# Kernel tuning notes

Measured on AMD Instinct MI355X. Metric: run time of the kernel, lower is better.

## Reference

```python
import jax, jax.numpy as jnp
import numpy as np

H = 8          # num_heads
CHUNK = 68     # tokens_per_chunk = blocks_per_chunk(4) * tokens_per_block(17)
EPS = 1e-5


def _layer_norm(t, w, b):
    m = t.mean(-1, keepdims=True)
    v = t.var(-1, keepdims=True)
    return (t - m) / jnp.sqrt(v + EPS) * w + b


def _forward(tokens, embedding, Wq, bq, Wk, bk, Wv, bv, Wg, bg, Wo, bo,
             gn_w, gn_b, ln1_w, ln1_b, ln2_w, ln2_b, w1, b1, w2, b2):
    B, S = tokens.shape
    L, D, _ = Wq.shape
    dh = D // H
    n_chunks = S // CHUNK

    x = embedding[tokens]  # [B,S,D]

    # per-head decay gammas (standard RetNet)
    gamma = 1.0 - 2.0 ** (-5.0 - jnp.arange(H, dtype=jnp.float32))  # [H]

    # rotary relative-position tables (absolute positions, fresh state n=0)
    pos = jnp.arange(S, dtype=jnp.float32)
    inv = 1.0 / (10000.0 ** (jnp.arange(0, dh, 2, dtype=jnp.float32) / dh))
    ang = pos[:, None] * inv[None, :]                      # [S, dh/2]
    cs = jnp.concatenate([jnp.cos(ang)] * 2, -1)[None, :, None, :]  # [1,S,1,dh]
    sn = jnp.concatenate([jnp.sin(ang)] * 2, -1)[None, :, None, :]

    def rot(t):  # t: [B,S,H,dh]
        t1, t2 = jnp.split(t, 2, axis=-1)
        return t * cs + jnp.concatenate([-t2, t1], -1) * sn

    # chunkwise decay structures
    idx = jnp.arange(CHUNK, dtype=jnp.float32)
    expo = idx[:, None] - idx[None, :]
    Dmask = jnp.where(expo >= 0, gamma[:, None, None] ** expo[None], 0.0)  # [H,C,C]
    cross_dec = gamma[None, :] ** (idx[:, None] + 1.0)          # [C,H]
    k_dec = gamma[None, :] ** (CHUNK - 1.0 - idx[:, None])      # [C,H]
    chunk_dec = gamma ** CHUNK                                  # [H]

    for l in range(L):
        h = _layer_norm(x, ln1_w[l], ln1_b[l])
        q = rot((h @ Wq[l] + bq[l]).reshape(B, S, H, dh))
        k = rot((h @ Wk[l] + bk[l]).reshape(B, S, H, dh)) * (dh ** -0.5)
        v = (h @ Wv[l] + bv[l]).reshape(B, S, H, dh)
        # split into chunks, scan carries the per-head KV state [B,H,dh,dh]
        qc = q.reshape(B, n_chunks, CHUNK, H, dh).transpose(1, 0, 2, 3, 4)
        kc = k.reshape(B, n_chunks, CHUNK, H, dh).transpose(1, 0, 2, 3, 4)
        vc = v.reshape(B, n_chunks, CHUNK, H, dh).transpose(1, 0, 2, 3, 4)

        def step(state, qkv):
            qq, kk, vv = qkv  # each [B,C,H,dh]
            inner = jnp.einsum('bihd,bjhd->bhij', qq, kk) * Dmask
            out = jnp.einsum('bhij,bjhd->bihd', inner, vv)
            out = out + jnp.einsum('bihd,bhde->bihe', qq, state) * cross_dec[None, :, :, None]
            state = state * chunk_dec[None, :, None, None] + \
                jnp.einsum('bjhd,bjhe->bhde', kk * k_dec[None, :, :, None], vv)
            return state, out

        state0 = jnp.zeros((B, H, dh, dh), dtype=x.dtype)
        _, ret = jax.lax.scan(step, state0, (qc, kc, vc))
        ret = ret.transpose(1, 0, 2, 3, 4).reshape(B, S, H, dh)
        # per-head group norm
        m = ret.mean(-1, keepdims=True)
        vr = ret.var(-1, keepdims=True)
        ret = (ret - m) / jnp.sqrt(vr + EPS)
        ret = (ret * gn_w[l].reshape(H, dh) + gn_b[l].reshape(H, dh)).reshape(B, S, D)
        g = jax.nn.silu(h @ Wg[l] + bg[l])
        x = x + (g * ret) @ Wo[l] + bo[l]
        h2 = _layer_norm(x, ln2_w[l], ln2_b[l])
        x = x + jax.nn.silu(h2 @ w1[l] + b1[l]) @ w2[l] + b2[l]
    return x


def setup_inputs() -> dict:
    key = jax.random.key(0)
    B, S, D, L, FF, V = 16, 408, 512, 10, 2048, 519
    ks = jax.random.split(key, 16)
    r = lambda i, shape, s=0.02: jax.random.normal(ks[i], shape, dtype=jnp.float32) * s
    return {
        'tokens': jax.random.randint(ks[0], (B, S), 0, V, dtype=jnp.int32),
        'embedding': r(1, (V, D)),
        'Wq': r(2, (L, D, D)), 'bq': jnp.zeros((L, D), jnp.float32),
        'Wk': r(3, (L, D, D)), 'bk': jnp.zeros((L, D), jnp.float32),
        'Wv': r(4, (L, D, D)), 'bv': jnp.zeros((L, D), jnp.float32),
        'Wg': r(5, (L, D, D)), 'bg': jnp.zeros((L, D), jnp.float32),
        'Wo': r(6, (L, D, D)), 'bo': jnp.zeros((L, D), jnp.float32),
        'gn_w': jnp.ones((L, D), jnp.float32), 'gn_b': jnp.zeros((L, D), jnp.float32),
        'ln1_w': jnp.ones((L, D), jnp.float32), 'ln1_b': jnp.zeros((L, D), jnp.float32),
        'ln2_w': jnp.ones((L, D), jnp.float32), 'ln2_b': jnp.zeros((L, D), jnp.float32),
        'w1': r(7, (L, D, FF)), 'b1': jnp.zeros((L, FF), jnp.float32),
        'w2': r(8, (L, FF, D)), 'b2': jnp.zeros((L, D), jnp.float32),
    }


def reference(tokens, embedding, Wq, bq, Wk, bk, Wv, bv, Wg, bg, Wo, bo,
              gn_w, gn_b, ln1_w, ln1_b, ln2_w, ln2_b, w1, b1, w2, b2):
    return _forward(tokens, embedding, Wq, bq, Wk, bk, Wv, bv, Wg, bg, Wo, bo,
                    gn_w, gn_b, ln1_w, ln1_b, ln2_w, ln2_b, w1, b1, w2, b2)
```

## Files before the change

kernel.cpp:

```cpp
#include <hip/hip_runtime.h>
#include <hip/hip_bf16.h>

#define H 8
#define DH 64
#define DMODEL 512
#define SEQ 408
#define BATCH 16
#define NLAYER 10
#define FFDIM 2048
#define CHUNK 68
#define NCHUNK 6
#define M (BATCH*SEQ)
#define EPS 1e-5f

typedef __hip_bfloat16 bf16;
typedef unsigned short ushort_t;
typedef short bf8v __attribute__((ext_vector_type(8)));
typedef float f4v  __attribute__((ext_vector_type(4)));

static constexpr size_t QKVG_STRIDE = 2u*512*512;
static constexpr size_t QKVG_HL     = 512*512;
static constexpr size_t WO_HI = 0;
static constexpr size_t WO_LO = WO_HI + 512*512;
static constexpr size_t W1_HI = WO_LO + 512*512;
static constexpr size_t W1_LO = W1_HI + 2048*512;
static constexpr size_t W2_HI = W1_LO + 2048*512;
static constexpr size_t W2_LO = W2_HI + 512*2048;

__device__ __forceinline__ float us2f(unsigned short u){ return __uint_as_float(((unsigned)u) << 16); }
__device__ __forceinline__ unsigned short f2bfs(float f){
  __bf16 h = (__bf16)f;
  return *(unsigned short*)&h;
}
__device__ __forceinline__ void split2(float f, unsigned short& hi, unsigned short& lo){
  hi = f2bfs(f);
  lo = f2bfs(f - us2f(hi));
}

typedef const __attribute__((address_space(1))) unsigned int* gas_ptr;
typedef __attribute__((address_space(3))) unsigned int* las_ptr;
__device__ __forceinline__ void gld16(const void* g, void* l){
  __builtin_amdgcn_global_load_lds((gas_ptr)g, (las_ptr)l, 16, 0, 0);
}

__device__ __forceinline__ int xcd_swz(int fid, int nwg){
  int q = nwg >> 3;
  return (fid & 7) * q + (fid >> 3);
}

__global__ void embed_kernel(const int* __restrict__ tokens, const float* __restrict__ emb,
                             float* __restrict__ x){
  int idx = blockIdx.x*256 + threadIdx.x;
  if (idx >= M*DMODEL) return;
  int r = idx >> 9; int d = idx & 511;
  x[idx] = emb[(size_t)tokens[r]*DMODEL + d];
}

__global__ __launch_bounds__(256) void ln_kernel(const float* __restrict__ x,
    const float* __restrict__ w, const float* __restrict__ b,
    ushort_t* __restrict__ hhi, ushort_t* __restrict__ hlo){
  __shared__ float red[8];
  int r = blockIdx.x, tid = threadIdx.x;
  size_t base = (size_t)r*DMODEL;
  float v0 = x[base + tid], v1 = x[base + tid + 256];
  float s = v0 + v1, s2 = v0*v0 + v1*v1;
  int lane = tid & 63, wv = tid >> 6;
  #pragma unroll
  for (int o = 32; o; o >>= 1){ s += __shfl_xor(s, o); s2 += __shfl_xor(s2, o); }
  if (lane == 0){ red[wv] = s; red[wv+4] = s2; }
  __syncthreads();
  float tot  = red[0]+red[1]+red[2]+red[3];
  float tot2 = red[4]+red[5]+red[6]+red[7];
  float mean = tot * (1.0f/512.0f);
  float var  = tot2 * (1.0f/512.0f) - mean*mean;
  float rinv = rsqrtf(var + EPS);
  float o0 = (v0-mean)*rinv*w[tid]     + b[tid];
  float o1 = (v1-mean)*rinv*w[tid+256] + b[tid+256];
  unsigned short hi, lo;
  split2(o0, hi, lo); hhi[base+tid] = hi; hlo[base+tid] = lo;
  split2(o1, hi, lo); hhi[base+tid+256] = hi; hlo[base+tid+256] = lo;
}

__device__ __forceinline__ void wsplit_tile(const float* __restrict__ W,
    ushort_t* __restrict__ hi, ushort_t* __restrict__ lo,
    int N, int K, int n0, int k0)
{
  __shared__ float tb[32][33];
  int tx = threadIdx.x & 31, ty = threadIdx.x >> 5;
  #pragma unroll
  for (int r = 0; r < 32; r += 8)
    tb[ty+r][tx] = W[(size_t)(k0+ty+r)*N + n0 + tx];
  __syncthreads();
  #pragma unroll
  for (int r = 0; r < 32; r += 8){
    float v = tb[tx][ty+r];
    unsigned short h, l; split2(v, h, l);
    size_t o = (size_t)(n0+ty+r)*K + k0 + tx;
    hi[o] = h; lo[o] = l;
  }
}

__global__ __launch_bounds__(256) void wsplit_qkvg_kernel(
    const float* __restrict__ Wq, const float* __restrict__ Wk,
    const float* __restrict__ Wv, const float* __restrict__ Wg,
    ushort_t* __restrict__ wsp)
{
  int z = blockIdx.z;
  const float* W = (z==0)?Wq:(z==1)?Wk:(z==2)?Wv:Wg;
  ushort_t* hi = wsp + (size_t)z*QKVG_STRIDE;
  wsplit_tile(W, hi, hi + QKVG_HL, 512, 512, blockIdx.x*32, blockIdx.y*32);
}

__global__ __launch_bounds__(256) void wsplit_ffo_kernel(
    const float* __restrict__ Wo, const float* __restrict__ w1,
    const float* __restrict__ w2, ushort_t* __restrict__ wsp)
{
  int b = blockIdx.x;
  const float* W; ushort_t* hi; int N, K, n0, k0;
  if (b < 256){
    W = Wo; hi = wsp + WO_HI; N = 512; K = 512;
    n0 = (b & 15)*32; k0 = (b >> 4)*32;
  } else if (b < 1280){
    int bb = b - 256;
    W = w1; hi = wsp + W1_HI; N = 2048; K = 512;
    n0 = (bb & 63)*32; k0 = (bb >> 6)*32;
  } else {
    int bb = b - 1280;
    W = w2; hi = wsp + W2_HI; N = 512; K = 2048;
    n0 = (bb & 15)*32; k0 = (bb >> 4)*32;
  }
  wsplit_tile(W, hi, hi + (size_t)N*K, N, K, n0, k0);
}

#define BK 32

#define STAGE_PS(buf, kofs) do{ \
    gld16(aHp + (kofs), &AsH[buf][tid*8]); \
    gld16(aLp + (kofs), &AsL[buf][tid*8]); \
    gld16(bHp + (kofs), &BsH[buf][tid*8]); \
    gld16(bLp + (kofs), &BsL[buf][tid*8]); \
    gld16(bHp2 + (kofs), &BsH[buf][tid*8 + 2048]); \
    gld16(bLp2 + (kofs), &BsL[buf][tid*8 + 2048]); \
  }while(0)

__global__ __launch_bounds__(256) void gemm_ps_kernel(
    const ushort_t* __restrict__ Ahi, const ushort_t* __restrict__ Alo,
    const ushort_t* __restrict__ Bhi, const ushort_t* __restrict__ Blo,
    const float* __restrict__ bias,
    const float* Cin, float* Cout, ushort_t* Co_hi, ushort_t* Co_lo,
    int N, int K, int epi)
{
  __shared__ __align__(16) short AsH[2][64*BK];
  __shared__ __align__(16) short AsL[2][64*BK];
  __shared__ __align__(16) short BsH[2][128*BK];
  __shared__ __align__(16) short BsL[2][128*BK];
  int tid = threadIdx.x;
  int lane = tid & 63, wave = tid >> 6;
  int wm = (wave >> 1) * 32, wn = (wave & 1) * 64;
  int l15 = lane & 15, quad = lane >> 4;

  int nwg = gridDim.x * gridDim.y;
  int fid = blockIdx.y * gridDim.x + blockIdx.x;
  int swz = xcd_swz(fid, nwg);
  int bn = (swz % gridDim.x) * 128;
  int bm = (swz / gridDim.x) * 64;

  f4v acc[2][4];
  #pragma unroll
  for (int i = 0; i < 2; i++)
    #pragma unroll
    for (int j = 0; j < 4; j++) acc[i][j] = (f4v){0.f,0.f,0.f,0.f};

  int arow = tid >> 2, ak = (tid & 3) * 8;
  const ushort_t* aHp  = Ahi + (size_t)(bm + arow)*K + ak;
  const ushort_t* aLp  = Alo + (size_t)(bm + arow)*K + ak;
  const ushort_t* bHp  = Bhi + (size_t)(bn + arow)*K + ak;
  const ushort_t* bLp  = Blo + (size_t)(bn + arow)*K + ak;
  const ushort_t* bHp2 = Bhi + (size_t)(bn + 64 + arow)*K + ak;
  const ushort_t* bLp2 = Blo + (size_t)(bn + 64 + arow)*K + ak;

  STAGE_PS(0, 0);
  const int nt = K / BK;
  for (int t = 0; t < nt; t++){
    __syncthreads();
    if (t + 1 < nt) STAGE_PS((t+1)&1, (t+1)*BK);
    int cur = t & 1;
    bf8v afh[2], afl[2], bfh[4], bfl[4];
    #pragma unroll
    for (int i = 0; i < 2; i++){
      afh[i] = *(const bf8v*)&AsH[cur][(wm + i*16 + l15)*BK + quad*8];
      afl[i] = *(const bf8v*)&AsL[cur][(wm + i*16 + l15)*BK + quad*8];
    }
    #pragma unroll
    for (int j = 0; j < 4; j++){
      bfh[j] = *(const bf8v*)&BsH[cur][(wn + j*16 + l15)*BK + quad*8];
      bfl[j] = *(const bf8v*)&BsL[cur][(wn + j*16 + l15)*BK + quad*8];
    }
    #pragma unroll
    for (int i = 0; i < 2; i++)
      #pragma unroll
      for (int j = 0; j < 4; j++){
        acc[i][j] = __builtin_amdgcn_mfma_f32_16x16x32_bf16(afh[i], bfl[j], acc[i][j], 0, 0, 0);
        acc[i][j] = __builtin_amdgcn_mfma_f32_16x16x32_bf16(afl[i], bfh[j], acc[i][j], 0, 0, 0);
        acc[i][j] = __builtin_amdgcn_mfma_f32_16x16x32_bf16(afh[i], bfh[j], acc[i][j], 0, 0, 0);
      }
  }
  #pragma unroll
  for (int i = 0; i < 2; i++){
    int m0 = bm + wm + i*16 + quad*4;
    #pragma unroll
    for (int j = 0; j < 4; j++){
      int n = bn + wn + j*16 + l15;
      float bsv = bias[n];
      #pragma unroll
      for (int r = 0; r < 4; r++){
        int m = m0 + r;
        float c = acc[i][j][r] + bsv;
        if (epi == 1) c = c / (1.0f + expf(-c));
        if (epi == 2) c += Cin[(size_t)m*N + n];
        if (Co_hi){
          unsigned short hi, lo; split2(c, hi, lo);
          Co_hi[(size_t)m*N + n] = hi;
          Co_lo[(size_t)m*N + n] = lo;
        } else {
          Cout[(size_t)m*N + n] = c;
        }
      }
    }
  }
}

__global__ __launch_bounds__(256) void gemm_qkvg_kernel(
    const ushort_t* __restrict__ Ahi, const ushort_t* __restrict__ Alo,
    const ushort_t* __restrict__ wsp,
    const float* __restrict__ bq, const float* __restrict__ bk,
    const float* __restrict__ bv, const float* __restrict__ bg,
    float* __restrict__ qo, float* __restrict__ ko,
    float* __restrict__ vo, float* __restrict__ go)
{
  const int N = DMODEL, K = DMODEL;
  __shared__ __align__(16) short AsH[2][64*BK];
  __shared__ __align__(16) short AsL[2][64*BK];
  __shared__ __align__(16) short BsH[2][128*BK];
  __shared__ __align__(16) short BsL[2][128*BK];
  int tid = threadIdx.x;
  int lane = tid & 63, wave = tid >> 6;
  int wm = (wave >> 1) * 32, wn = (wave & 1) * 64;
  int l15 = lane & 15, quad = lane >> 4;

  int nwg = gridDim.x * gridDim.y;
  int fid = blockIdx.y * gridDim.x + blockIdx.x;
  int swz = xcd_swz(fid, nwg);
  int bx = swz % gridDim.x;
  int which = bx >> 2;
  int bn = (bx & 3) * 128;
  int bm = (swz / gridDim.x) * 64;

  const ushort_t* Bhi = wsp + (size_t)which * QKVG_STRIDE;
  const ushort_t* Blo = Bhi + QKVG_HL;
  const float* bias = (which==0) ? bq : (which==1) ? bk : (which==2) ? bv : bg;
  float* out        = (which==0) ? qo : (which==1) ? ko : (which==2) ? vo : go;

  f4v acc[2][4];
  #pragma unroll
  for (int i = 0; i < 2; i++)
    #pragma unroll
    for (int j = 0; j < 4; j++) acc[i][j] = (f4v){0.f,0.f,0.f,0.f};

  int arow = tid >> 2, ak = (tid & 3) * 8;
  const ushort_t* aHp  = Ahi + (size_t)(bm + arow)*K + ak;
  const ushort_t* aLp  = Alo + (size_t)(bm + arow)*K + ak;
  const ushort_t* bHp  = Bhi + (size_t)(bn + arow)*K + ak;
  const ushort_t* bLp  = Blo + (size_t)(bn + arow)*K + ak;
  const ushort_t* bHp2 = Bhi + (size_t)(bn + 64 + arow)*K + ak;
  const ushort_t* bLp2 = Blo + (size_t)(bn + 64 + arow)*K + ak;

  STAGE_PS(0, 0);
  const int nt = K / BK;
  for (int t = 0; t < nt; t++){
    __syncthreads();
    if (t + 1 < nt) STAGE_PS((t+1)&1, (t+1)*BK);
    int cur = t & 1;
    bf8v afh[2], afl[2], bfh[4], bfl[4];
    #pragma unroll
    for (int i = 0; i < 2; i++){
      afh[i] = *(const bf8v*)&AsH[cur][(wm + i*16 + l15)*BK + quad*8];
      afl[i] = *(const bf8v*)&AsL[cur][(wm + i*16 + l15)*BK + quad*8];
    }
    #pragma unroll
    for (int j = 0; j < 4; j++){
      bfh[j] = *(const bf8v*)&BsH[cur][(wn + j*16 + l15)*BK + quad*8];
      bfl[j] = *(const bf8v*)&BsL[cur][(wn + j*16 + l15)*BK + quad*8];
    }
    #pragma unroll
    for (int i = 0; i < 2; i++)
      #pragma unroll
      for (int j = 0; j < 4; j++){
        acc[i][j] = __builtin_amdgcn_mfma_f32_16x16x32_bf16(afh[i], bfl[j], acc[i][j], 0, 0, 0);
        acc[i][j] = __builtin_amdgcn_mfma_f32_16x16x32_bf16(afl[i], bfh[j], acc[i][j], 0, 0, 0);
        acc[i][j] = __builtin_amdgcn_mfma_f32_16x16x32_bf16(afh[i], bfh[j], acc[i][j], 0, 0, 0);
      }
  }
  #pragma unroll
  for (int i = 0; i < 2; i++){
    int m0 = bm + wm + i*16 + quad*4;
    #pragma unroll
    for (int j = 0; j < 4; j++){
      int n = bn + wn + j*16 + l15;
      float bsv = bias[n];
      #pragma unroll
      for (int r = 0; r < 4; r++){
        int m = m0 + r;
        float c = acc[i][j][r] + bsv;
        if (which == 3) c = c / (1.0f + expf(-c));
        out[(size_t)m*N + n] = c;
      }
    }
  }
}

__global__ void rope_kernel(float* __restrict__ q, float* __restrict__ k){
  int idx = blockIdx.x*256 + threadIdx.x;
  if (idx >= M*256) return;
  int r = idx >> 8, p = idx & 255;
  int hh = p >> 5, i = p & 31;
  int s = r % SEQ;
  float inv = powf(10000.0f, -(float)(2*i) * (1.0f/64.0f));
  float ang = (float)s * inv;
  float sn, c; sincosf(ang, &sn, &c);
  size_t base = (size_t)r*DMODEL + hh*64 + i;
  float q1 = q[base], q2 = q[base+32];
  q[base]    = q1*c - q2*sn;
  q[base+32] = q2*c + q1*sn;
  float k1 = k[base], k2 = k[base+32];
  const float sc = 0.125f;
  k[base]    = (k1*c - k2*sn)*sc;
  k[base+32] = (k2*c + k1*sn)*sc;
}

__global__ __launch_bounds__(256) void ret_chunkkv_kernel(
    const float* __restrict__ k, const float* __restrict__ v, float* __restrict__ Ast)
{
  __shared__ __align__(16) float kT[DH][CHUNK];
  __shared__ __align__(16) float vs[CHUNK][DH];
  __shared__ float gpw[CHUNK];
  int tid = threadIdx.x;
  int c = blockIdx.x % NCHUNK;
  int bh = blockIdx.x / NCHUNK;
  int hh = bh & 7, b = bh >> 3;
  float gamma = 1.0f - exp2f(-5.0f - (float)hh);
  if (tid < CHUNK) gpw[tid] = powf(gamma, (float)(CHUNK-1-tid));
  size_t rowbase = ((size_t)(b*SEQ + c*CHUNK))*DMODEL + hh*DH;
  for (int e = tid; e < CHUNK*DH; e += 256){
    int i = e >> 6, d = e & 63;
    size_t g = rowbase + (size_t)i*DMODEL + d;
    kT[d][i] = k[g];
    vs[i][d] = v[g];
  }
  __syncthreads();
  float* A = Ast + (size_t)blockIdx.x * (DH*DH);
  for (int e = tid; e < DH*16; e += 256){
    int d = e >> 4, q4 = (e & 15) * 4;
    float4 a4 = {0,0,0,0};
    for (int j = 0; j < CHUNK; j++){
      float kj = kT[d][j] * gpw[j];
      float4 v4 = *(const float4*)&vs[j][q4];
      a4.x += kj*v4.x; a4.y += kj*v4.y; a4.z += kj*v4.z; a4.w += kj*v4.w;
    }
    *(float4*)&A[d*DH + q4] = a4;
  }
}

__global__ __launch_bounds__(256) void ret_scan_kernel(float* __restrict__ Ast)
{
  int bh = blockIdx.x, hh = bh & 7;
  float gamma = 1.0f - exp2f(-5.0f - (float)hh);
  float chdec = powf(gamma, (float)CHUNK);
  int tid = threadIdx.x;
  float4 run[4];
  #pragma unroll
  for (int t = 0; t < 4; t++) run[t] = (float4){0,0,0,0};
  size_t base = (size_t)bh * NCHUNK * (DH*DH) + (size_t)tid*16;
  for (int c = 0; c < NCHUNK; c++){
    float4* slot = (float4*)(Ast + base + (size_t)c*(DH*DH));
    float4 a[4];
    #pragma unroll
    for (int t = 0; t < 4; t++) a[t] = slot[t];
    #pragma unroll
    for (int t = 0; t < 4; t++) slot[t] = run[t];
    #pragma unroll
    for (int t = 0; t < 4; t++){
      run[t].x = run[t].x*chdec + a[t].x;
      run[t].y = run[t].y*chdec + a[t].y;
      run[t].z = run[t].z*chdec + a[t].z;
      run[t].w = run[t].w*chdec + a[t].w;
    }
  }
}

__global__ __launch_bounds__(256) void ret_out_kernel(
    const float* __restrict__ q, const float* __restrict__ k, const float* __restrict__ v,
    const float* __restrict__ Ast, float* __restrict__ ret)
{
  __shared__ __align__(16) float qs[CHUNK][DH];
  __shared__ __align__(16) float kT[DH][CHUNK];
  __shared__ __align__(16) float vs[CHUNK][DH];
  __shared__ __align__(16) float sts[DH*DH];
  __shared__ float inner[34][CHUNK];
  __shared__ float gpw[CHUNK];
  int tid = threadIdx.x;
  int c = blockIdx.x % NCHUNK;
  int bh = blockIdx.x / NCHUNK;
  int hh = bh & 7, b = bh >> 3;
  float gamma = 1.0f - exp2f(-5.0f - (float)hh);
  if (tid < CHUNK) gpw[tid] = powf(gamma, (float)tid);
  size_t rowbase = ((size_t)(b*SEQ + c*CHUNK))*DMODEL + hh*DH;
  for (int e = tid; e < CHUNK*DH; e += 256){
    int i = e >> 6, d = e & 63;
    size_t g = rowbase + (size_t)i*DMODEL + d;
    qs[i][d] = q[g];
    kT[d][i] = k[g];
    vs[i][d] = v[g];
  }
  const float* st = Ast + (size_t)blockIdx.x * (DH*DH);
  for (int e = tid*4; e < DH*DH; e += 1024)
    *(float4*)&sts[e] = *(const float4*)&st[e];
  __syncthreads();
  for (int p = 0; p < 2; p++){
    int i0 = p*34;
    for (int e = tid; e < 34*CHUNK; e += 256){
      int ii = e / CHUNK, j = e - ii*CHUNK;
      int i = i0 + ii;
      float val = 0.0f;
      if (j <= i){
        float dot = 0.0f;
        #pragma unroll 16
        for (int d = 0; d < DH; d++) dot += qs[i][d] * kT[d][j];
        val = dot * gpw[i-j];
      }
      inner[ii][j] = val;
    }
    __syncthreads();
    for (int e = tid; e < 34*16; e += 256){
      int ii = e >> 4, q4 = (e & 15) * 4;
      int i = i0 + ii;
      float4 o4 = {0,0,0,0};
      for (int j = 0; j <= i; j++){
        float w = inner[ii][j];
        float4 v4 = *(const float4*)&vs[j][q4];
        o4.x += w*v4.x; o4.y += w*v4.y; o4.z += w*v4.z; o4.w += w*v4.w;
      }
      float4 c4 = {0,0,0,0};
      #pragma unroll 8
      for (int e2 = 0; e2 < DH; e2++){
        float qv = qs[i][e2];
        float4 s4 = *(const float4*)&sts[e2*DH + q4];
        c4.x += qv*s4.x; c4.y += qv*s4.y; c4.z += qv*s4.z; c4.w += qv*s4.w;
      }
      float cd = gpw[i] * gamma;
      size_t ob = rowbase + (size_t)i*DMODEL + q4;
      float4 o; o.x = o4.x + cd*c4.x; o.y = o4.y + cd*c4.y;
      o.z = o4.z + cd*c4.z; o.w = o4.w + cd*c4.w;
      *(float4*)&ret[ob] = o;
    }
    __syncthreads();
  }
}

__global__ __launch_bounds__(512) void gnorm_gate_kernel(const float* __restrict__ ret,
    const float* __restrict__ g, const float* __restrict__ gnw, const float* __restrict__ gnb,
    ushort_t* __restrict__ ohi, ushort_t* __restrict__ olo)
{
  int r = blockIdx.x, tid = threadIdx.x;
  size_t idx = (size_t)r*DMODEL + tid;
  float val = ret[idx];
  float s = val, s2 = val*val;
  #pragma unroll
  for (int o = 32; o; o >>= 1){ s += __shfl_xor(s, o); s2 += __shfl_xor(s2, o); }
  float mean = s * (1.0f/64.0f);
  float var  = s2 * (1.0f/64.0f) - mean*mean;
  float y = (val - mean) * rsqrtf(var + EPS);
  y = y * gnw[tid] + gnb[tid];
  y = y * g[idx];
  unsigned short hi, lo; split2(y, hi, lo);
  ohi[idx] = hi; olo[idx] = lo;
}

__global__ void outwrite_kernel(const float* __restrict__ x, float* __restrict__ out){
  int idx = blockIdx.x*256 + threadIdx.x;
  if (idx < M*DMODEL) out[idx] = x[idx];
}

extern "C" void kernel_launch(void* const* d_in, const int* in_sizes, int n_in,
                              void* d_out, int out_size, void* d_ws, size_t ws_size,
                              hipStream_t stream)
{
  (void)in_sizes; (void)n_in; (void)out_size; (void)ws_size;
  const int*   tokens = (const int*)d_in[0];
  const float* emb  = (const float*)d_in[1];
  const float* Wq = (const float*)d_in[2];  const float* bq = (const float*)d_in[3];
  const float* Wk = (const float*)d_in[4];  const float* bk = (const float*)d_in[5];
  const float* Wv = (const float*)d_in[6];  const float* bv = (const float*)d_in[7];
  const float* Wg = (const float*)d_in[8];  const float* bg = (const float*)d_in[9];
  const float* Wo = (const float*)d_in[10]; const float* bo = (const float*)d_in[11];
  const float* gnw = (const float*)d_in[12]; const float* gnb = (const float*)d_in[13];
  const float* ln1w = (const float*)d_in[14]; const float* ln1b = (const float*)d_in[15];
  const float* ln2w = (const float*)d_in[16]; const float* ln2b = (const float*)d_in[17];
  const float* w1 = (const float*)d_in[18]; const float* b1 = (const float*)d_in[19];
  const float* w2 = (const float*)d_in[20]; const float* b2 = (const float*)d_in[21];

  const size_t MD = (size_t)M*DMODEL;
  float* xf = (float*)d_ws;
  float* qf = xf + MD;
  float* kf = qf + MD;
  float* vf = kf + MD;
  float* gf = vf + MD;
  float* rf = gf + MD;
  ushort_t* h_hi = (ushort_t*)(rf + MD);
  ushort_t* h_lo = h_hi + MD;
  float* Ast = (float*)h_hi;
  ushort_t* rg_hi = h_hi;
  ushort_t* rg_lo = h_lo;
  ushort_t* ff_hi = (ushort_t*)qf;
  ushort_t* ff_lo = (ushort_t*)vf;
  ushort_t* wsp = (ushort_t*)rf;

  embed_kernel<<<(M*DMODEL)/256, 256, 0, stream>>>(tokens, emb, xf);

  dim3 gqkvg(16, M/64);
  dim3 g512(DMODEL/128, M/64);
  dim3 gff(FFDIM/128, M/64);
  dim3 gsplit4(16, 16, 4);
  for (int l = 0; l < NLAYER; l++){
    const size_t wO = (size_t)l*DMODEL*DMODEL;
    const size_t bO = (size_t)l*DMODEL;
    const size_t w1O = (size_t)l*DMODEL*FFDIM;
    const size_t b1O = (size_t)l*FFDIM;
    wsplit_qkvg_kernel<<<gsplit4, 256, 0, stream>>>(Wq + wO, Wk + wO, Wv + wO, Wg + wO, wsp);
    ln_kernel<<<M, 256, 0, stream>>>(xf, ln1w + bO, ln1b + bO, h_hi, h_lo);
    gemm_qkvg_kernel<<<gqkvg, 256, 0, stream>>>(h_hi, h_lo, wsp,
        bq + bO, bk + bO, bv + bO, bg + bO,
        qf, kf, vf, gf);
    rope_kernel<<<M, 256, 0, stream>>>(qf, kf);
    ret_chunkkv_kernel<<<BATCH*H*NCHUNK, 256, 0, stream>>>(kf, vf, Ast);
    ret_scan_kernel<<<BATCH*H, 256, 0, stream>>>(Ast);
    ret_out_kernel<<<BATCH*H*NCHUNK, 256, 0, stream>>>(qf, kf, vf, Ast, rf);
    gnorm_gate_kernel<<<M, 512, 0, stream>>>(rf, gf, gnw + bO, gnb + bO, rg_hi, rg_lo);
    wsplit_ffo_kernel<<<2304, 256, 0, stream>>>(Wo + wO, w1 + w1O, w2 + w1O, wsp);
    gemm_ps_kernel<<<g512, 256, 0, stream>>>(rg_hi, rg_lo,
        wsp + WO_HI, wsp + WO_LO, bo + bO, xf, xf, nullptr, nullptr, DMODEL, DMODEL, 2);
    ln_kernel<<<M, 256, 0, stream>>>(xf, ln2w + bO, ln2b + bO, h_hi, h_lo);
    gemm_ps_kernel<<<gff, 256, 0, stream>>>(h_hi, h_lo,
        wsp + W1_HI, wsp + W1_LO, b1 + b1O, nullptr, nullptr, ff_hi, ff_lo, FFDIM, DMODEL, 1);
    gemm_ps_kernel<<<g512, 256, 0, stream>>>(ff_hi, ff_lo,
        wsp + W2_HI, wsp + W2_LO, b2 + bO, xf, xf, nullptr, nullptr, DMODEL, FFDIM, 2);
  }
  outwrite_kernel<<<(M*DMODEL)/256, 256, 0, stream>>>(xf, (float*)d_out);
}
```

Measured before the change: 3.767 ms.

## Deepen GEMM prefetch to two tiles and use 64-wide N tiles for 512-out GEMMs

Restructures the bf16-split GEMM main loops so two K-tiles are in flight. Explicit vmcnt waits and split barriers let the next-next tile load while the current tile computes, replacing a single sync per iteration. The output-projection and FFN-down GEMMs are templated to use a 64-column N tile, which doubles their workgroup count for better occupancy and CU fill. This adds a second barrier per iteration and relies on hand-counted vmcnt values that must match the number of issued loads.

```diff
diff --git a/kernel.cpp b/kernel.cpp
--- a/kernel.cpp
+++ b/kernel.cpp
@@ -134,15 +134,7 @@
 
 #define BK 32
 
-#define STAGE_PS(buf, kofs) do{ \
-    gld16(aHp + (kofs), &AsH[buf][tid*8]); \
-    gld16(aLp + (kofs), &AsL[buf][tid*8]); \
-    gld16(bHp + (kofs), &BsH[buf][tid*8]); \
-    gld16(bLp + (kofs), &BsL[buf][tid*8]); \
-    gld16(bHp2 + (kofs), &BsH[buf][tid*8 + 2048]); \
-    gld16(bLp2 + (kofs), &BsL[buf][tid*8 + 2048]); \
-  }while(0)
-
+template<int TBN>
 __global__ __launch_bounds__(256) void gemm_ps_kernel(
     const ushort_t* __restrict__ Ahi, const ushort_t* __restrict__ Alo,
     const ushort_t* __restrict__ Bhi, const ushort_t* __restrict__ Blo,
@@ -150,26 +142,27 @@
     const float* Cin, float* Cout, ushort_t* Co_hi, ushort_t* Co_lo,
     int N, int K, int epi)
 {
+  constexpr int TNW = TBN/32;
   __shared__ __align__(16) short AsH[2][64*BK];
   __shared__ __align__(16) short AsL[2][64*BK];
-  __shared__ __align__(16) short BsH[2][128*BK];
-  __shared__ __align__(16) short BsL[2][128*BK];
+  __shared__ __align__(16) short BsH[2][TBN*BK];
+  __shared__ __align__(16) short BsL[2][TBN*BK];
   int tid = threadIdx.x;
   int lane = tid & 63, wave = tid >> 6;
-  int wm = (wave >> 1) * 32, wn = (wave & 1) * 64;
+  int wm = (wave >> 1) * 32, wn = (wave & 1) * (TBN/2);
   int l15 = lane & 15, quad = lane >> 4;
 
   int nwg = gridDim.x * gridDim.y;
   int fid = blockIdx.y * gridDim.x + blockIdx.x;
   int swz = xcd_swz(fid, nwg);
-  int bn = (swz % gridDim.x) * 128;
+  int bn = (swz % gridDim.x) * TBN;
   int bm = (swz / gridDim.x) * 64;
 
-  f4v acc[2][4];
+  f4v acc[2][TNW];
   #pragma unroll
   for (int i = 0; i < 2; i++)
     #pragma unroll
-    for (int j = 0; j < 4; j++) acc[i][j] = (f4v){0.f,0.f,0.f,0.f};
+    for (int j = 0; j < TNW; j++) acc[i][j] = (f4v){0.f,0.f,0.f,0.f};
 
   int arow = tid >> 2, ak = (tid & 3) * 8;
   const ushort_t* aHp  = Ahi + (size_t)(bm + arow)*K + ak;
@@ -179,37 +172,59 @@
   const ushort_t* bHp2 = Bhi + (size_t)(bn + 64 + arow)*K + ak;
   const ushort_t* bLp2 = Blo + (size_t)(bn + 64 + arow)*K + ak;
 
-  STAGE_PS(0, 0);
+  auto STAGE = [&](int buf, int kofs){
+    gld16(aHp + kofs, &AsH[buf][tid*8]);
+    gld16(aLp + kofs, &AsL[buf][tid*8]);
+    gld16(bHp + kofs, &BsH[buf][tid*8]);
+    gld16(bLp + kofs, &BsL[buf][tid*8]);
+    if constexpr (TBN == 128){
+      gld16(bHp2 + kofs, &BsH[buf][tid*8 + 2048]);
+      gld16(bLp2 + kofs, &BsL[buf][tid*8 + 2048]);
+    }
+  };
+
+  STAGE(0, 0);
+  STAGE(1, BK);
   const int nt = K / BK;
   for (int t = 0; t < nt; t++){
-    __syncthreads();
-    if (t + 1 < nt) STAGE_PS((t+1)&1, (t+1)*BK);
+    if (t + 1 < nt){
+      if constexpr (TBN == 128) asm volatile("s_waitcnt vmcnt(6)" ::: "memory");
+      else                      asm volatile("s_waitcnt vmcnt(4)" ::: "memory");
+    } else {
+      asm volatile("s_waitcnt vmcnt(0)" ::: "memory");
+    }
+    __builtin_amdgcn_s_barrier();
+    asm volatile("" ::: "memory");
     int cur = t & 1;
-    bf8v afh[2], afl[2], bfh[4], bfl[4];
+    bf8v afh[2], afl[2], bfh[TNW], bfl[TNW];
     #pragma unroll
     for (int i = 0; i < 2; i++){
       afh[i] = *(const bf8v*)&AsH[cur][(wm + i*16 + l15)*BK + quad*8];
       afl[i] = *(const bf8v*)&AsL[cur][(wm + i*16 + l15)*BK + quad*8];
     }
     #pragma unroll
-    for (int j = 0; j < 4; j++){
+    for (int j = 0; j < TNW; j++){
       bfh[j] = *(const bf8v*)&BsH[cur][(wn + j*16 + l15)*BK + quad*8];
       bfl[j] = *(const bf8v*)&BsL[cur][(wn + j*16 + l15)*BK + quad*8];
     }
     #pragma unroll
     for (int i = 0; i < 2; i++)
       #pragma unroll
-      for (int j = 0; j < 4; j++){
+      for (int j = 0; j < TNW; j++){
         acc[i][j] = __builtin_amdgcn_mfma_f32_16x16x32_bf16(afh[i], bfl[j], acc[i][j], 0, 0, 0);
         acc[i][j] = __builtin_amdgcn_mfma_f32_16x16x32_bf16(afl[i], bfh[j], acc[i][j], 0, 0, 0);
         acc[i][j] = __builtin_amdgcn_mfma_f32_16x16x32_bf16(afh[i], bfh[j], acc[i][j], 0, 0, 0);
       }
+    asm volatile("s_waitcnt lgkmcnt(0)" ::: "memory");
+    __builtin_amdgcn_s_barrier();
+    asm volatile("" ::: "memory");
+    if (t + 2 < nt) STAGE(cur, (t+2)*BK);
   }
   #pragma unroll
   for (int i = 0; i < 2; i++){
     int m0 = bm + wm + i*16 + quad*4;
     #pragma unroll
-    for (int j = 0; j < 4; j++){
+    for (int j = 0; j < TNW; j++){
       int n = bn + wn + j*16 + l15;
       float bsv = bias[n];
       #pragma unroll
@@ -275,11 +290,23 @@
   const ushort_t* bHp2 = Bhi + (size_t)(bn + 64 + arow)*K + ak;
   const ushort_t* bLp2 = Blo + (size_t)(bn + 64 + arow)*K + ak;
 
-  STAGE_PS(0, 0);
+  auto STAGE = [&](int buf, int kofs){
+    gld16(aHp + kofs, &AsH[buf][tid*8]);
+    gld16(aLp + kofs, &AsL[buf][tid*8]);
+    gld16(bHp + kofs, &BsH[buf][tid*8]);
+    gld16(bLp + kofs, &BsL[buf][tid*8]);
+    gld16(bHp2 + kofs, &BsH[buf][tid*8 + 2048]);
+    gld16(bLp2 + kofs, &BsL[buf][tid*8 + 2048]);
+  };
+
+  STAGE(0, 0);
+  STAGE(1, BK);
   const int nt = K / BK;
   for (int t = 0; t < nt; t++){
-    __syncthreads();
-    if (t + 1 < nt) STAGE_PS((t+1)&1, (t+1)*BK);
+    if (t + 1 < nt) asm volatile("s_waitcnt vmcnt(6)" ::: "memory");
+    else            asm volatile("s_waitcnt vmcnt(0)" ::: "memory");
+    __builtin_amdgcn_s_barrier();
+    asm volatile("" ::: "memory");
     int cur = t & 1;
     bf8v afh[2], afl[2], bfh[4], bfl[4];
     #pragma unroll
@@ -300,6 +327,10 @@
         acc[i][j] = __builtin_amdgcn_mfma_f32_16x16x32_bf16(afl[i], bfh[j], acc[i][j], 0, 0, 0);
         acc[i][j] = __builtin_amdgcn_mfma_f32_16x16x32_bf16(afh[i], bfh[j], acc[i][j], 0, 0, 0);
       }
+    asm volatile("s_waitcnt lgkmcnt(0)" ::: "memory");
+    __builtin_amdgcn_s_barrier();
+    asm volatile("" ::: "memory");
+    if (t + 2 < nt) STAGE(cur, (t+2)*BK);
   }
   #pragma unroll
   for (int i = 0; i < 2; i++){
@@ -528,7 +559,7 @@
   embed_kernel<<<(M*DMODEL)/256, 256, 0, stream>>>(tokens, emb, xf);
 
   dim3 gqkvg(16, M/64);
-  dim3 g512(DMODEL/128, M/64);
+  dim3 g512(DMODEL/64, M/64);
   dim3 gff(FFDIM/128, M/64);
   dim3 gsplit4(16, 16, 4);
   for (int l = 0; l < NLAYER; l++){
@@ -547,12 +578,12 @@
     ret_out_kernel<<<BATCH*H*NCHUNK, 256, 0, stream>>>(qf, kf, vf, Ast, rf);
     gnorm_gate_kernel<<<M, 512, 0, stream>>>(rf, gf, gnw + bO, gnb + bO, rg_hi, rg_lo);
     wsplit_ffo_kernel<<<2304, 256, 0, stream>>>(Wo + wO, w1 + w1O, w2 + w1O, wsp);
-    gemm_ps_kernel<<<g512, 256, 0, stream>>>(rg_hi, rg_lo,
+    gemm_ps_kernel<64><<<g512, 256, 0, stream>>>(rg_hi, rg_lo,
         wsp + WO_HI, wsp + WO_LO, bo + bO, xf, xf, nullptr, nullptr, DMODEL, DMODEL, 2);
     ln_kernel<<<M, 256, 0, stream>>>(xf, ln2w + bO, ln2b + bO, h_hi, h_lo);
-    gemm_ps_kernel<<<gff, 256, 0, stream>>>(h_hi, h_lo,
+    gemm_ps_kernel<128><<<gff, 256, 0, stream>>>(h_hi, h_lo,
         wsp + W1_HI, wsp + W1_LO, b1 + b1O, nullptr, nullptr, ff_hi, ff_lo, FFDIM, DMODEL, 1);
-    gemm_ps_kernel<<<g512, 256, 0, stream>>>(ff_hi, ff_lo,
+    gemm_ps_kernel<64><<<g512, 256, 0, stream>>>(ff_hi, ff_lo,
         wsp + W2_HI, wsp + W2_LO, b2 + bO, xf, xf, nullptr, nullptr, DMODEL, FFDIM, 2);
   }
   outwrite_kernel<<<(M*DMODEL)/256, 256, 0, stream>>>(xf, (float*)d_out);
```

New measurement: 3.747 ms. No clear change (-0.5%).
